# Optimization experiments

Hardware: AMD Instinct MI355X
Metric: run time of the kernel (lower is better)

## Reference

```python
import jax, jax.numpy as jnp
import numpy as np

B, N, DIM = 4, 1024, 512
H, DH = 16, 13            # dim_head stays at Attention's default 13
INNER = H * DH            # 208
L = 2                     # depth
MULT = 4
LA, LG = 1.0, 0.5
EPS = 1e-5


def layer_norm(x, g, b):
    m = jnp.mean(x, axis=-1, keepdims=True)
    v = jnp.mean((x - m) ** 2, axis=-1, keepdims=True)
    return (x - m) / jnp.sqrt(v + EPS) * g + b


def attention(x, mask, adj, qkv_w, out_w, out_b):
    b, n, _ = x.shape
    qkv = (x @ qkv_w).reshape(b, n, H, 3, DH)          # 'b n (h qkv d)'
    q = jnp.transpose(qkv[..., 0, :], (0, 2, 1, 3))    # b h n d
    k = jnp.transpose(qkv[..., 1, :], (0, 2, 1, 3))
    v = jnp.transpose(qkv[..., 2, :], (0, 2, 1, 3))
    dots = jnp.einsum('bhid,bhjd->bhij', q, k) * (DH ** -0.5)
    m2 = mask[:, None, :, None] & mask[:, None, None, :]  # b 1 n n
    big = jnp.finfo(dots.dtype).max
    dots = jnp.where(m2, dots, -big)
    adj4 = jnp.where(m2, adj[:, None, :, :], 0.0)
    attn = jax.nn.softmax(dots, axis=-1) * LA + LG * adj4
    out = jnp.einsum('bhij,bhjd->bhid', attn, v)
    out = jnp.transpose(out, (0, 2, 1, 3)).reshape(b, n, INNER)
    return out @ out_w + out_b


def feed_forward(x, w1, b1, w2, b2):
    return jax.nn.gelu(x @ w1 + b1, approximate=False) @ w2 + b2


def setup_inputs() -> dict:
    key = jax.random.key(0)
    ks = jax.random.split(key, 24)
    s = 0.02
    inp = {
        'x': jax.random.normal(ks[0], (B, N, DIM), jnp.float32),
        'mask': jax.random.randint(ks[1], (B, N), 0, 2).astype(bool),
        'adjacency_mat': jax.random.uniform(ks[2], (B, N, N), jnp.float32),
        'embed_w': jax.random.normal(ks[3], (DIM, DIM), jnp.float32) * s,
        'embed_b': jnp.zeros((DIM,), jnp.float32),
        'ln1_g': jnp.ones((L, DIM), jnp.float32),
        'ln1_b': jnp.zeros((L, DIM), jnp.float32),
        'qkv_w': jax.random.normal(ks[4], (L, DIM, 3 * INNER), jnp.float32) * s,
        'out_w': jax.random.normal(ks[5], (L, INNER, DIM), jnp.float32) * s,
        'out_b': jnp.zeros((L, DIM), jnp.float32),
        'ln2_g': jnp.ones((L, DIM), jnp.float32),
        'ln2_b': jnp.zeros((L, DIM), jnp.float32),
        'ff1_w': jax.random.normal(ks[6], (L, DIM, MULT * DIM), jnp.float32) * s,
        'ff1_b': jnp.zeros((L, MULT * DIM), jnp.float32),
        'ff2_w': jax.random.normal(ks[7], (L, MULT * DIM, DIM), jnp.float32) * s,
        'ff2_b': jnp.zeros((L, DIM), jnp.float32),
        'lnout_g': jnp.ones((DIM,), jnp.float32),
        'lnout_b': jnp.zeros((DIM,), jnp.float32),
        'ffo1_w': jax.random.normal(ks[8], (DIM, MULT * DIM), jnp.float32) * s,
        'ffo1_b': jnp.zeros((MULT * DIM,), jnp.float32),
        'ffo2_w': jax.random.normal(ks[9], (MULT * DIM, DIM), jnp.float32) * s,
        'ffo2_b': jnp.zeros((DIM,), jnp.float32),
    }
    return inp


def reference(x, mask, adjacency_mat, embed_w, embed_b, ln1_g, ln1_b, qkv_w,
              out_w, out_b, ln2_g, ln2_b, ff1_w, ff1_b, ff2_w, ff2_b,
              lnout_g, lnout_b, ffo1_w, ffo1_b, ffo2_w, ffo2_b):
    h = x @ embed_w + embed_b
    for l in range(L):
        h = h + attention(layer_norm(h, ln1_g[l], ln1_b[l]), mask,
                          adjacency_mat, qkv_w[l], out_w[l], out_b[l])
        h = h + feed_forward(layer_norm(h, ln2_g[l], ln2_b[l]),
                             ff1_w[l], ff1_b[l], ff2_w[l], ff2_b[l])
    h = layer_norm(h, lnout_g, lnout_b)
    h = jnp.mean(h, axis=-2)                     # pool over nodes -> [B, DIM]
    return feed_forward(h, ffo1_w, ffo1_b, ffo2_w, ffo2_b)
```

## Files before the change

### kernel.cpp

```cpp
#include <hip/hip_runtime.h>
#include <math.h>

#define BB    4
#define NN    1024
#define DIM   512
#define HH    16
#define DH    13
#define INNER 208
#define QKVN  624
#define QKVNP 640
#define KOUTP 224
#define FFH   2048
#define ROWS  4096

typedef __attribute__((ext_vector_type(8))) short short8v;
typedef __attribute__((ext_vector_type(4))) float f32x4;

__device__ __forceinline__ unsigned short f2bf(float f) {
    union { float f; unsigned int u; } x; x.f = f;
    unsigned int u = x.u + 0x7FFFu + ((x.u >> 16) & 1u);
    return (unsigned short)(u >> 16);
}
__device__ __forceinline__ float gelu_exact(float x) {
    return 0.5f * x * (1.0f + erff(x * 0.70710678118654752f));
}

__global__ __launch_bounds__(1024) void mask_detect_kernel(
        const unsigned char* __restrict__ mraw, int* __restrict__ flag) {
    __shared__ int any;
    if (threadIdx.x == 0) any = 0;
    __syncthreads();
    int t = threadIdx.x;
    int v = mraw[4 * t + 1] | mraw[4 * t + 2] | mraw[4 * t + 3];
    if (v) atomicOr(&any, 1);
    __syncthreads();
    if (threadIdx.x == 0) *flag = any;
}

__global__ __launch_bounds__(256) void mask_convert_kernel(
        const void* __restrict__ mraw, const int* __restrict__ flag,
        int* __restrict__ rowmask, float* __restrict__ maskfb) {
    int i = blockIdx.x * 256 + threadIdx.x;
    int v;
    if (*flag) v = ((const unsigned char*)mraw)[i] != 0;
    else       v = ((const int*)mraw)[i] != 0;
    rowmask[i] = v;
    maskfb[i] = v ? 1.0f : 0.0f;
}

__global__ __launch_bounds__(256) void zero16_kernel(uint4* __restrict__ p) {
    p[blockIdx.x * 256 + threadIdx.x] = (uint4){0u, 0u, 0u, 0u};
}

__global__ __launch_bounds__(256) void convw_kernel(
        const float* __restrict__ src, unsigned short* __restrict__ dst,
        int srcK, int srcN, int dstK, int dstN) {
    __shared__ float t[64][65];
    const int n0 = blockIdx.x * 64, k0 = blockIdx.y * 64;
    const int tq = threadIdx.x & 15, tr = threadIdx.x >> 4;
#pragma unroll
    for (int it = 0; it < 4; ++it) {
        int kl = tr + it * 16;
        int kg = k0 + kl;
        int ng = n0 + tq * 4;
        float4 v = {0.f, 0.f, 0.f, 0.f};
        if (kg < srcK) {
            const float* sp = src + (size_t)kg * srcN;
            if (ng + 3 < srcN) v = *(const float4*)(sp + ng);
            else {
                if (ng + 0 < srcN) v.x = sp[ng + 0];
                if (ng + 1 < srcN) v.y = sp[ng + 1];
                if (ng + 2 < srcN) v.z = sp[ng + 2];
                if (ng + 3 < srcN) v.w = sp[ng + 3];
            }
        }
        t[kl][tq * 4 + 0] = v.x; t[kl][tq * 4 + 1] = v.y;
        t[kl][tq * 4 + 2] = v.z; t[kl][tq * 4 + 3] = v.w;
    }
    __syncthreads();
#pragma unroll
    for (int it = 0; it < 4; ++it) {
        int nl = tr + it * 16;
        int ng = n0 + nl;
        int kg = k0 + tq * 4;
        if (ng < dstN && kg < dstK) {
            ushort4 o;
            o.x = f2bf(t[tq * 4 + 0][nl]); o.y = f2bf(t[tq * 4 + 1][nl]);
            o.z = f2bf(t[tq * 4 + 2][nl]); o.w = f2bf(t[tq * 4 + 3][nl]);
            *(ushort4*)(dst + (size_t)ng * dstK + kg) = o;
        }
    }
}

__global__ __launch_bounds__(256) void convx_kernel(
        const float* __restrict__ src, unsigned short* __restrict__ dst, int n8) {
    int idx = blockIdx.x * 256 + threadIdx.x;
    if (idx >= n8) return;
    float4 a = ((const float4*)src)[idx * 2];
    float4 b = ((const float4*)src)[idx * 2 + 1];
    uint4 o;
    o.x = (unsigned)f2bf(a.x) | ((unsigned)f2bf(a.y) << 16);
    o.y = (unsigned)f2bf(a.z) | ((unsigned)f2bf(a.w) << 16);
    o.z = (unsigned)f2bf(b.x) | ((unsigned)f2bf(b.y) << 16);
    o.w = (unsigned)f2bf(b.z) | ((unsigned)f2bf(b.w) << 16);
    ((uint4*)dst)[idx] = o;
}

__global__ __launch_bounds__(256) void zpad_kernel(unsigned short* __restrict__ attnout) {
    int idx = blockIdx.x * 256 + threadIdx.x;
    int row = idx >> 4, c = INNER + (idx & 15);
    attnout[(size_t)row * KOUTP + c] = 0;
}

__global__ __launch_bounds__(256) void adjmask_kernel(
        const float* __restrict__ adj, const int* __restrict__ rmask,
        unsigned short* __restrict__ adjbf) {
    int idx = blockIdx.x * 256 + threadIdx.x;
    int j8 = idx & 127;
    int row = idx >> 7;
    int b = row >> 10;
    int mi = rmask[row];
    const float* ap = adj + (size_t)row * NN + j8 * 8;
    const int* rm = rmask + (b << 10) + j8 * 8;
    float4 a0 = *(const float4*)ap, a1 = *(const float4*)(ap + 4);
    unsigned short o[8];
    o[0] = (mi && rm[0]) ? f2bf(a0.x) : 0;
    o[1] = (mi && rm[1]) ? f2bf(a0.y) : 0;
    o[2] = (mi && rm[2]) ? f2bf(a0.z) : 0;
    o[3] = (mi && rm[3]) ? f2bf(a0.w) : 0;
    o[4] = (mi && rm[4]) ? f2bf(a1.x) : 0;
    o[5] = (mi && rm[5]) ? f2bf(a1.y) : 0;
    o[6] = (mi && rm[6]) ? f2bf(a1.z) : 0;
    o[7] = (mi && rm[7]) ? f2bf(a1.w) : 0;
    uint4 pk;
    pk.x = (unsigned)o[0] | ((unsigned)o[1] << 16);
    pk.y = (unsigned)o[2] | ((unsigned)o[3] << 16);
    pk.z = (unsigned)o[4] | ((unsigned)o[5] << 16);
    pk.w = (unsigned)o[6] | ((unsigned)o[7] << 16);
    *(uint4*)(adjbf + (size_t)row * NN + j8 * 8) = pk;
}

template<int EPI, int BM, int BN>
__global__ __launch_bounds__(256) void mm_kernel(
        const unsigned short* __restrict__ A, const unsigned short* __restrict__ W,
        const float* __restrict__ bias, void* __restrict__ Cdst,
        int K, int lda, int ldc,
        long long aBatch, long long bBatch, long long cBatch,
        unsigned short* __restrict__ Qb, unsigned short* __restrict__ Kb,
        unsigned short* __restrict__ Vtb, unsigned short* __restrict__ V2t)
{
    constexpr int MF = BM / 32;
    constexpr int NF = BN / 32;
    constexpr int AROUNDS = BM / 64;
    constexpr int BROUNDS = BN / 64;
    __shared__ unsigned short As[BM * 32];
    __shared__ unsigned short Bs[BN * 32];
    const int tid = threadIdx.x;
    const int m0 = blockIdx.y * BM;
    const int n0 = blockIdx.x * BN;
    const int z  = blockIdx.z;

    const int lane = tid & 63;
    const int wv = tid >> 6;
    const int wvbase = wv << 6;
    const int wm = wv >> 1, wn = wv & 1;
    const int lrow = lane & 15, kgrp = lane >> 4;

    f32x4 acc[MF][NF];
#pragma unroll
    for (int i = 0; i < MF; ++i)
#pragma unroll
        for (int j = 0; j < NF; ++j) acc[i][j] = (f32x4){0.f, 0.f, 0.f, 0.f};

    const unsigned short* Ab = A + (size_t)z * aBatch;
    const unsigned short* Wb = W + (size_t)z * bBatch;

    for (int k0 = 0; k0 < K; k0 += 32) {
#pragma unroll
        for (int r = 0; r < AROUNDS; ++r) {
            int c = r * 256 + tid;
            const unsigned short* g = Ab + (size_t)(m0 + (c >> 2)) * lda + k0 + (c & 3) * 8;
            __builtin_amdgcn_global_load_lds((const unsigned int*)g,
                (unsigned int*)&As[(r * 256 + wvbase) * 8], 16, 0, 0);
        }
#pragma unroll
        for (int r = 0; r < BROUNDS; ++r) {
            int c = r * 256 + tid;
            const unsigned short* g = Wb + (size_t)(n0 + (c >> 2)) * K + k0 + (c & 3) * 8;
            __builtin_amdgcn_global_load_lds((const unsigned int*)g,
                (unsigned int*)&Bs[(r * 256 + wvbase) * 8], 16, 0, 0);
        }
        __syncthreads();
        short8v af[MF], bfv[NF];
#pragma unroll
        for (int f = 0; f < MF; ++f)
            af[f] = *(const short8v*)&As[(wm * (BM / 2) + f * 16 + lrow) * 32 + kgrp * 8];
#pragma unroll
        for (int f = 0; f < NF; ++f)
            bfv[f] = *(const short8v*)&Bs[(wn * (BN / 2) + f * 16 + lrow) * 32 + kgrp * 8];
#pragma unroll
        for (int fi = 0; fi < MF; ++fi)
#pragma unroll
            for (int fj = 0; fj < NF; ++fj)
                acc[fi][fj] = __builtin_amdgcn_mfma_f32_16x16x32_bf16(
                    af[fi], bfv[fj], acc[fi][fj], 0, 0, 0);
        __syncthreads();
    }

#pragma unroll
    for (int fi = 0; fi < MF; ++fi) {
#pragma unroll
        for (int fj = 0; fj < NF; ++fj) {
#pragma unroll
            for (int p = 0; p < 4; ++p) {
                int row = m0 + wm * (BM / 2) + fi * 16 + kgrp * 4 + p;
                int col = n0 + wn * (BN / 2) + fj * 16 + lrow;
                float v = acc[fi][fj][p];
                if (EPI == 0) {
                    float* C = (float*)Cdst + (size_t)z * cBatch;
                    if (bias) v += bias[col];
                    C[(size_t)row * ldc + col] = v;
                } else if (EPI == 1) {
                    unsigned short* C = (unsigned short*)Cdst;
                    C[(size_t)row * ldc + col] = f2bf(gelu_exact(v + bias[col]));
                } else if (EPI == 2) {
                    float* C = (float*)Cdst;
                    C[(size_t)row * ldc + col] += v + bias[col];
                } else {
                    if (col < QKVN) {
                        int hh  = col / 39;
                        int rem = col - hh * 39;
                        int sel = rem / 13;
                        int d   = rem - sel * 13;
                        int bb = row >> 10, n = row & (NN - 1);
                        int bh = bb * HH + hh;
                        unsigned short bv = f2bf(v);
                        if (sel == 0) {
                            Qb[((size_t)bh * NN + n) * 16 + d] = bv;
                        } else if (sel == 1) {
                            int rr = (n & ~31) | (((n >> 2) & 1) << 4)
                                   | (((n >> 3) & 3) << 2) | (n & 3);
                            Kb[((size_t)bh * NN + rr) * 16 + d] = bv;
                        } else {
                            Vtb[((size_t)bh * 16 + d) * NN + n] = bv;
                            V2t[((size_t)bb * 256 + hh * 13 + d) * NN + n] = bv;
                        }
                    }
                }
            }
        }
    }
}

template<int BFOUT>
__global__ __launch_bounds__(256) void ln_kernel(
        const float* __restrict__ x, const float* __restrict__ g,
        const float* __restrict__ bta, void* __restrict__ y) {
    const int lane = threadIdx.x & 63;
    const int row = (blockIdx.x * 256 + threadIdx.x) >> 6;
    const float* xp = x + (size_t)row * DIM + lane * 8;
    float4 v0 = *(const float4*)(xp);
    float4 v1 = *(const float4*)(xp + 4);
    float s = v0.x + v0.y + v0.z + v0.w + v1.x + v1.y + v1.z + v1.w;
#pragma unroll
    for (int off = 32; off >= 1; off >>= 1) s += __shfl_xor(s, off);
    float mean = s * (1.0f / DIM);
    float q =
        (v0.x - mean) * (v0.x - mean) + (v0.y - mean) * (v0.y - mean) +
        (v0.z - mean) * (v0.z - mean) + (v0.w - mean) * (v0.w - mean) +
        (v1.x - mean) * (v1.x - mean) + (v1.y - mean) * (v1.y - mean) +
        (v1.z - mean) * (v1.z - mean) + (v1.w - mean) * (v1.w - mean);
#pragma unroll
    for (int off = 32; off >= 1; off >>= 1) q += __shfl_xor(q, off);
    float rstd = rsqrtf(q * (1.0f / DIM) + 1e-5f);
    const int c = lane * 8;
    float4 g0 = *(const float4*)(g + c), g1 = *(const float4*)(g + c + 4);
    float4 b0 = *(const float4*)(bta + c), b1 = *(const float4*)(bta + c + 4);
    float o0 = (v0.x - mean) * rstd * g0.x + b0.x;
    float o1 = (v0.y - mean) * rstd * g0.y + b0.y;
    float o2 = (v0.z - mean) * rstd * g0.z + b0.z;
    float o3 = (v0.w - mean) * rstd * g0.w + b0.w;
    float o4 = (v1.x - mean) * rstd * g1.x + b1.x;
    float o5 = (v1.y - mean) * rstd * g1.y + b1.y;
    float o6 = (v1.z - mean) * rstd * g1.z + b1.z;
    float o7 = (v1.w - mean) * rstd * g1.w + b1.w;
    if (BFOUT) {
        unsigned short* yp = (unsigned short*)y + (size_t)row * DIM + c;
        uint4 o;
        o.x = (unsigned)f2bf(o0) | ((unsigned)f2bf(o1) << 16);
        o.y = (unsigned)f2bf(o2) | ((unsigned)f2bf(o3) << 16);
        o.z = (unsigned)f2bf(o4) | ((unsigned)f2bf(o5) << 16);
        o.w = (unsigned)f2bf(o6) | ((unsigned)f2bf(o7) << 16);
        *(uint4*)yp = o;
    } else {
        float* yp = (float*)y + (size_t)row * DIM + c;
        *(float4*)(yp)     = (float4){o0, o1, o2, o3};
        *(float4*)(yp + 4) = (float4){o4, o5, o6, o7};
    }
}

__global__ __launch_bounds__(256) void attn4_kernel(
        const unsigned short* __restrict__ Qb, const unsigned short* __restrict__ Kb,
        const unsigned short* __restrict__ Vtb, const float* __restrict__ adjout,
        const int* __restrict__ rmask, const float* __restrict__ maskfb,
        unsigned short* __restrict__ attnout) {
    const int tid = threadIdx.x;
    const int qt = blockIdx.x, h = blockIdx.y, b = blockIdx.z;
    const int bh = b * HH + h;
    const int wv = tid >> 6, lane = tid & 63;
    const int lrow = lane & 15, g = lane >> 4;
    const int q = qt * 64 + wv * 16 + lrow;
    const int mi = rmask[b * NN + q];
    const float scl = mi ? (0.27735009811261457f * 1.4426950408889634f) : 0.0f;
    const float mif = mi ? 1.0f : 0.0f;

    short8v qf = (short8v){0, 0, 0, 0, 0, 0, 0, 0};
    if (g < 2)
        qf = *(const short8v*)(Qb + ((size_t)bh * NN + q) * 16 + g * 8);

    const unsigned short* Kbh = Kb + (size_t)bh * NN * 16;
    const unsigned short* Vrow = Vtb + ((size_t)bh * 16 + lrow) * NN;
    const float* mfp = maskfb + b * NN;

    f32x4 oacc = (f32x4){0.f, 0.f, 0.f, 0.f};
    float zacc = 0.0f;

    for (int t = 0; t < 32; ++t) {
        const int j0 = t * 32;
        short8v kf0 = (short8v){0, 0, 0, 0, 0, 0, 0, 0};
        short8v kf1 = (short8v){0, 0, 0, 0, 0, 0, 0, 0};
        if (g < 2) {
            kf0 = *(const short8v*)(Kbh + (size_t)(j0 + lrow) * 16 + g * 8);
            kf1 = *(const short8v*)(Kbh + (size_t)(j0 + 16 + lrow) * 16 + g * 8);
        }
        f32x4 s0 = (f32x4){0.f, 0.f, 0.f, 0.f};
        f32x4 s1 = (f32x4){0.f, 0.f, 0.f, 0.f};
        s0 = __builtin_amdgcn_mfma_f32_16x16x32_bf16(kf0, qf, s0, 0, 0, 0);
        s1 = __builtin_amdgcn_mfma_f32_16x16x32_bf16(kf1, qf, s1, 0, 0, 0);
        float4 m0 = *(const float4*)&mfp[j0 + g * 8];
        float4 m1 = *(const float4*)&mfp[j0 + g * 8 + 4];
        float w0 = exp2f(fminf(s0[0] * scl, 80.f)) * fmaf(mif, m0.x - 1.f, 1.f);
        float w1 = exp2f(fminf(s0[1] * scl, 80.f)) * fmaf(mif, m0.y - 1.f, 1.f);
        float w2 = exp2f(fminf(s0[2] * scl, 80.f)) * fmaf(mif, m0.z - 1.f, 1.f);
        float w3 = exp2f(fminf(s0[3] * scl, 80.f)) * fmaf(mif, m0.w - 1.f, 1.f);
        float w4 = exp2f(fminf(s1[0] * scl, 80.f)) * fmaf(mif, m1.x - 1.f, 1.f);
        float w5 = exp2f(fminf(s1[1] * scl, 80.f)) * fmaf(mif, m1.y - 1.f, 1.f);
        float w6 = exp2f(fminf(s1[2] * scl, 80.f)) * fmaf(mif, m1.z - 1.f, 1.f);
        float w7 = exp2f(fminf(s1[3] * scl, 80.f)) * fmaf(mif, m1.w - 1.f, 1.f);
        zacc += ((w0 + w1) + (w2 + w3)) + ((w4 + w5) + (w6 + w7));
        unsigned p01, p23, p45, p67;
        asm("v_cvt_pk_bf16_f32 %0, %1, %2" : "=v"(p01) : "v"(w0), "v"(w1));
        asm("v_cvt_pk_bf16_f32 %0, %1, %2" : "=v"(p23) : "v"(w2), "v"(w3));
        asm("v_cvt_pk_bf16_f32 %0, %1, %2" : "=v"(p45) : "v"(w4), "v"(w5));
        asm("v_cvt_pk_bf16_f32 %0, %1, %2" : "=v"(p67) : "v"(w6), "v"(w7));
        union { uint4 u4; short8v s8; } pu;
        pu.u4 = (uint4){p01, p23, p45, p67};
        short8v vf = *(const short8v*)(Vrow + j0 + g * 8);
        oacc = __builtin_amdgcn_mfma_f32_16x16x32_bf16(vf, pu.s8, oacc, 0, 0, 0);
    }

    zacc += __shfl_xor(zacc, 16);
    zacc += __shfl_xor(zacc, 32);
    float inv = 1.0f / zacc;

    const float* arow = adjout + ((size_t)(b * NN + q)) * 256 + h * 13;
    unsigned short* orow = attnout + (size_t)(b * NN + q) * KOUTP + h * 13;
#pragma unroll
    for (int p = 0; p < 4; ++p) {
        int d = 4 * g + p;
        if (d < 13)
            orow[d] = f2bf(fmaf(oacc[p], inv, 0.5f * arow[d]));
    }
}

__global__ __launch_bounds__(256) void pool1_kernel(
        const float* __restrict__ xn, float* __restrict__ poolpart) {
    __shared__ float red[256][4];
    const int ch = blockIdx.x, b = blockIdx.y;
    const int c4 = threadIdx.x & 127, p = threadIdx.x >> 7;
    const float* base = xn + ((size_t)(b * NN) + ch * 64 + p) * DIM + c4 * 4;
    float4 s = {0.f, 0.f, 0.f, 0.f};
    for (int r = 0; r < 32; ++r) {
        float4 v = *(const float4*)(base + (size_t)r * 2 * DIM);
        s.x += v.x; s.y += v.y; s.z += v.z; s.w += v.w;
    }
    *(float4*)red[threadIdx.x] = s;
    __syncthreads();
    if (threadIdx.x < 128) {
        float4 a = *(float4*)red[threadIdx.x];
        float4 c = *(float4*)red[threadIdx.x + 128];
        float4 o = {a.x + c.x, a.y + c.y, a.z + c.z, a.w + c.w};
        *(float4*)(poolpart + (size_t)(b * 16 + ch) * DIM + c4 * 4) = o;
    }
}

__global__ __launch_bounds__(256) void pool2_kernel(
        const float* __restrict__ poolpart, float* __restrict__ pooled) {
    int c = blockIdx.x * 256 + threadIdx.x;
    int b = c >> 9, col = c & 511;
    float s = 0.f;
    for (int ch = 0; ch < 16; ++ch)
        s += poolpart[(size_t)(b * 16 + ch) * DIM + col];
    pooled[c] = s * (1.0f / NN);
}

__global__ __launch_bounds__(256) void ffo1a_kernel(
        const float* __restrict__ pooled, const float* __restrict__ w,
        float* __restrict__ part) {
    int n = blockIdx.x * 256 + threadIdx.x;
    int kc = blockIdx.y;
    float s0 = 0.f, s1 = 0.f, s2 = 0.f, s3 = 0.f;
    for (int k = kc * 128; k < kc * 128 + 128; ++k) {
        float wv = w[(size_t)k * FFH + n];
        s0 = fmaf(pooled[k], wv, s0);
        s1 = fmaf(pooled[512 + k], wv, s1);
        s2 = fmaf(pooled[1024 + k], wv, s2);
        s3 = fmaf(pooled[1536 + k], wv, s3);
    }
    part[(size_t)(kc * 4 + 0) * FFH + n] = s0;
    part[(size_t)(kc * 4 + 1) * FFH + n] = s1;
    part[(size_t)(kc * 4 + 2) * FFH + n] = s2;
    part[(size_t)(kc * 4 + 3) * FFH + n] = s3;
}

__global__ __launch_bounds__(256) void ffo1b_kernel(
        const float* __restrict__ part, const float* __restrict__ bias,
        float* __restrict__ ffoh) {
    int c = blockIdx.x * 256 + threadIdx.x;
    int b = c >> 11, n = c & 2047;
    float s = bias[n];
#pragma unroll
    for (int kc = 0; kc < 4; ++kc)
        s += part[(size_t)(kc * 4 + b) * FFH + n];
    ffoh[c] = gelu_exact(s);
}

__global__ __launch_bounds__(256) void ffo2a_kernel(
        const float* __restrict__ ffoh, const float* __restrict__ w,
        float* __restrict__ part) {
    int n = blockIdx.x * 256 + threadIdx.x;
    int kc = blockIdx.y;
    float s0 = 0.f, s1 = 0.f, s2 = 0.f, s3 = 0.f;
    for (int k = kc * 128; k < kc * 128 + 128; ++k) {
        float wv = w[(size_t)k * DIM + n];
        s0 = fmaf(ffoh[k], wv, s0);
        s1 = fmaf(ffoh[2048 + k], wv, s1);
        s2 = fmaf(ffoh[4096 + k], wv, s2);
        s3 = fmaf(ffoh[6144 + k], wv, s3);
    }
    part[(size_t)(kc * 4 + 0) * DIM + n] = s0;
    part[(size_t)(kc * 4 + 1) * DIM + n] = s1;
    part[(size_t)(kc * 4 + 2) * DIM + n] = s2;
    part[(size_t)(kc * 4 + 3) * DIM + n] = s3;
}

__global__ __launch_bounds__(256) void ffo2b_kernel(
        const float* __restrict__ part, const float* __restrict__ bias,
        float* __restrict__ out) {
    int c = blockIdx.x * 256 + threadIdx.x;
    int b = c >> 9, n = c & 511;
    float s = bias[n];
#pragma unroll
    for (int kc = 0; kc < 16; ++kc)
        s += part[(size_t)(kc * 4 + b) * DIM + n];
    out[c] = s;
}

extern "C" void kernel_launch(void* const* d_in, const int* in_sizes, int n_in,
                              void* d_out, int out_size, void* d_ws, size_t ws_size,
                              hipStream_t stream) {
    const float* x       = (const float*)d_in[0];
    const void*  mraw    = d_in[1];
    const float* adj     = (const float*)d_in[2];
    const float* embed_w = (const float*)d_in[3];
    const float* embed_b = (const float*)d_in[4];
    const float* ln1_g   = (const float*)d_in[5];
    const float* ln1_b   = (const float*)d_in[6];
    const float* qkv_w   = (const float*)d_in[7];
    const float* out_w   = (const float*)d_in[8];
    const float* out_b   = (const float*)d_in[9];
    const float* ln2_g   = (const float*)d_in[10];
    const float* ln2_b   = (const float*)d_in[11];
    const float* ff1_w   = (const float*)d_in[12];
    const float* ff1_b   = (const float*)d_in[13];
    const float* ff2_w   = (const float*)d_in[14];
    const float* ff2_b   = (const float*)d_in[15];
    const float* lnout_g = (const float*)d_in[16];
    const float* lnout_b = (const float*)d_in[17];
    const float* ffo1_w  = (const float*)d_in[18];
    const float* ffo1_b  = (const float*)d_in[19];
    const float* ffo2_w  = (const float*)d_in[20];
    const float* ffo2_b  = (const float*)d_in[21];

    char* ws = (char*)d_ws;
    float*          h       = (float*)(ws + 0);
    unsigned short* xnbf    = (unsigned short*)(ws + 8388608);
    char*           R       = ws + 12582912;
    unsigned short* adjbf   = (unsigned short*)(R + 0);
    unsigned short* Qb      = (unsigned short*)(R + 8388608);
    unsigned short* Kb      = (unsigned short*)(R + 10485760);
    unsigned short* Vtb     = (unsigned short*)(R + 12582912);
    unsigned short* V2t     = (unsigned short*)(R + 14680064);
    float*          adjout  = (float*)(R + 16777216);
    unsigned short* ffh     = (unsigned short*)(R + 0);
    float*          xnf     = (float*)(R + 0);
    float*          part1   = (float*)(R + 8388608);
    float*          part2   = (float*)(R + 8519680);
    unsigned short* attnout = (unsigned short*)(ws + 37486592);
    unsigned short* embedwt = (unsigned short*)(ws + 39321600);
    unsigned short* qkvwt   = (unsigned short*)(ws + 39845888);
    unsigned short* outwt   = (unsigned short*)(ws + 41156608);
    unsigned short* ff1wt   = (unsigned short*)(ws + 41615360);
    unsigned short* ff2wt   = (unsigned short*)(ws + 45809664);
    float*          poolpart= (float*)(ws + 50003968);
    float*          pooled  = (float*)(ws + 50135040);
    float*          ffoh    = (float*)(ws + 50143232);
    int*            rowmask = (int*)(ws + 50176000);
    float*          maskfb  = (float*)(ws + 50192384);
    int*            flag    = (int*)(ws + 50208768);

    mask_detect_kernel<<<1, 1024, 0, stream>>>((const unsigned char*)mraw, flag);
    mask_convert_kernel<<<16, 256, 0, stream>>>(mraw, flag, rowmask, maskfb);
    convx_kernel<<<1024, 256, 0, stream>>>(x, xnbf, ROWS * DIM / 8);
    convw_kernel<<<dim3(8, 8), 256, 0, stream>>>(embed_w, embedwt, 512, 512, 512, 512);
    for (int l = 0; l < 2; ++l) {
        convw_kernel<<<dim3(10, 8), 256, 0, stream>>>(qkv_w + (size_t)l * 512 * 624,
            qkvwt + (size_t)l * QKVNP * 512, 512, 624, 512, QKVNP);
        convw_kernel<<<dim3(8, 4), 256, 0, stream>>>(out_w + (size_t)l * 208 * 512,
            outwt + (size_t)l * 512 * KOUTP, 208, 512, KOUTP, 512);
        convw_kernel<<<dim3(32, 8), 256, 0, stream>>>(ff1_w + (size_t)l * 512 * 2048,
            ff1wt + (size_t)l * 2048 * 512, 512, 2048, 512, 2048);
        convw_kernel<<<dim3(8, 32), 256, 0, stream>>>(ff2_w + (size_t)l * 512 * 2048,
            ff2wt + (size_t)l * 512 * 2048, 2048, 512, 2048, 512);
    }
    zpad_kernel<<<256, 256, 0, stream>>>(attnout);

    mm_kernel<0, 64, 64><<<dim3(8, 64, 1), 256, 0, stream>>>(
        xnbf, embedwt, embed_b, h, 512, 512, 512, 0, 0, 0,
        nullptr, nullptr, nullptr, nullptr);

    for (int l = 0; l < 2; ++l) {
        ln_kernel<1><<<1024, 256, 0, stream>>>(h, ln1_g + l * DIM, ln1_b + l * DIM, xnbf);
        zero16_kernel<<<2048, 256, 0, stream>>>((uint4*)(R + 8388608));
        mm_kernel<3, 128, 64><<<dim3(10, 32, 1), 256, 0, stream>>>(
            xnbf, qkvwt + (size_t)l * QKVNP * 512, nullptr, nullptr,
            512, 512, 0, 0, 0, 0, Qb, Kb, Vtb, V2t);
        adjmask_kernel<<<2048, 256, 0, stream>>>(adj, rowmask, adjbf);
        mm_kernel<0, 64, 64><<<dim3(4, 16, 4), 256, 0, stream>>>(
            adjbf, V2t, nullptr, adjout, 1024, 1024, 256,
            (long long)NN * NN, (long long)256 * NN, (long long)NN * 256,
            nullptr, nullptr, nullptr, nullptr);
        attn4_kernel<<<dim3(16, 16, 4), 256, 0, stream>>>(
            Qb, Kb, Vtb, adjout, rowmask, maskfb, attnout);
        mm_kernel<2, 64, 64><<<dim3(8, 64, 1), 256, 0, stream>>>(
            attnout, outwt + (size_t)l * 512 * KOUTP, out_b + l * DIM, h,
            KOUTP, KOUTP, 512, 0, 0, 0, nullptr, nullptr, nullptr, nullptr);
        ln_kernel<1><<<1024, 256, 0, stream>>>(h, ln2_g + l * DIM, ln2_b + l * DIM, xnbf);
        mm_kernel<1, 128, 128><<<dim3(16, 32, 1), 256, 0, stream>>>(
            xnbf, ff1wt + (size_t)l * 2048 * 512, ff1_b + l * FFH, ffh,
            512, 512, 2048, 0, 0, 0, nullptr, nullptr, nullptr, nullptr);
        mm_kernel<2, 64, 64><<<dim3(8, 64, 1), 256, 0, stream>>>(
            ffh, ff2wt + (size_t)l * 512 * 2048, ff2_b + l * DIM, h,
            2048, 2048, 512, 0, 0, 0, nullptr, nullptr, nullptr, nullptr);
    }

    ln_kernel<0><<<1024, 256, 0, stream>>>(h, lnout_g, lnout_b, xnf);
    pool1_kernel<<<dim3(16, 4), 256, 0, stream>>>(xnf, poolpart);
    pool2_kernel<<<8, 256, 0, stream>>>(poolpart, pooled);
    ffo1a_kernel<<<dim3(8, 4), 256, 0, stream>>>(pooled, ffo1_w, part1);
    ffo1b_kernel<<<32, 256, 0, stream>>>(part1, ffo1_b, ffoh);
    ffo2a_kernel<<<dim3(2, 16), 256, 0, stream>>>(ffoh, ffo2_w, part2);
    ffo2b_kernel<<<8, 256, 0, stream>>>(part2, ffo2_b, (float*)d_out);
}
```

Before: 400.1 us.

## Hoist adjacency masking and pad zeroing out of layer loop, shrink QKV tile

```diff
diff --git a/kernel.cpp b/kernel.cpp
--- a/kernel.cpp
+++ b/kernel.cpp
@@ -48,8 +48,27 @@
     maskfb[i] = v ? 1.0f : 0.0f;
 }
 
-__global__ __launch_bounds__(256) void zero16_kernel(uint4* __restrict__ p) {
-    p[blockIdx.x * 256 + threadIdx.x] = (uint4){0u, 0u, 0u, 0u};
+__global__ __launch_bounds__(256) void padzero_kernel(
+        unsigned short* __restrict__ Qb, unsigned short* __restrict__ Kb,
+        unsigned short* __restrict__ Vtb, unsigned short* __restrict__ V2t) {
+    int idx = blockIdx.x * 256 + threadIdx.x;
+    if (idx < 65536) {
+        unsigned short* p = Qb + (size_t)idx * 16 + 13;
+        p[0] = 0; p[1] = 0; p[2] = 0;
+    } else if (idx < 131072) {
+        unsigned short* p = Kb + (size_t)(idx - 65536) * 16 + 13;
+        p[0] = 0; p[1] = 0; p[2] = 0;
+    } else if (idx < 155648) {
+        int i = idx - 131072;
+        int bh = i / 384, r = (i >> 7) % 3, c = i & 127;
+        *(uint4*)(Vtb + ((size_t)(bh * 16 + 13 + r) * 1024 + c * 8)) =
+            (uint4){0u, 0u, 0u, 0u};
+    } else if (idx < 180224) {
+        int i = idx - 155648;
+        int b = i / 6144, r = (i >> 7) % 48, c = i & 127;
+        *(uint4*)(V2t + ((size_t)(b * 256 + 208 + r) * 1024 + c * 8)) =
+            (uint4){0u, 0u, 0u, 0u};
+    }
 }
 
 __global__ __launch_bounds__(256) void convw_kernel(
@@ -495,29 +514,28 @@
     char* ws = (char*)d_ws;
     float*          h       = (float*)(ws + 0);
     unsigned short* xnbf    = (unsigned short*)(ws + 8388608);
-    char*           R       = ws + 12582912;
-    unsigned short* adjbf   = (unsigned short*)(R + 0);
-    unsigned short* Qb      = (unsigned short*)(R + 8388608);
-    unsigned short* Kb      = (unsigned short*)(R + 10485760);
-    unsigned short* Vtb     = (unsigned short*)(R + 12582912);
-    unsigned short* V2t     = (unsigned short*)(R + 14680064);
-    float*          adjout  = (float*)(R + 16777216);
-    unsigned short* ffh     = (unsigned short*)(R + 0);
-    float*          xnf     = (float*)(R + 0);
-    float*          part1   = (float*)(R + 8388608);
-    float*          part2   = (float*)(R + 8519680);
-    unsigned short* attnout = (unsigned short*)(ws + 37486592);
-    unsigned short* embedwt = (unsigned short*)(ws + 39321600);
-    unsigned short* qkvwt   = (unsigned short*)(ws + 39845888);
-    unsigned short* outwt   = (unsigned short*)(ws + 41156608);
-    unsigned short* ff1wt   = (unsigned short*)(ws + 41615360);
-    unsigned short* ff2wt   = (unsigned short*)(ws + 45809664);
-    float*          poolpart= (float*)(ws + 50003968);
-    float*          pooled  = (float*)(ws + 50135040);
-    float*          ffoh    = (float*)(ws + 50143232);
-    int*            rowmask = (int*)(ws + 50176000);
-    float*          maskfb  = (float*)(ws + 50192384);
-    int*            flag    = (int*)(ws + 50208768);
+    unsigned short* adjbf   = (unsigned short*)(ws + 12582912);
+    unsigned short* Qb      = (unsigned short*)(ws + 20971520);
+    unsigned short* Kb      = (unsigned short*)(ws + 23068672);
+    unsigned short* Vtb     = (unsigned short*)(ws + 25165824);
+    unsigned short* V2t     = (unsigned short*)(ws + 27262976);
+    float*          adjout  = (float*)(ws + 29360128);
+    unsigned short* ffh     = (unsigned short*)(ws + 33554432);
+    float*          xnf     = (float*)(ws + 50331648);
+    unsigned short* attnout = (unsigned short*)(ws + 58720256);
+    unsigned short* embedwt = (unsigned short*)(ws + 60555264);
+    unsigned short* qkvwt   = (unsigned short*)(ws + 61079552);
+    unsigned short* outwt   = (unsigned short*)(ws + 62390272);
+    unsigned short* ff1wt   = (unsigned short*)(ws + 62849024);
+    unsigned short* ff2wt   = (unsigned short*)(ws + 67043328);
+    float*          poolpart= (float*)(ws + 71237632);
+    float*          pooled  = (float*)(ws + 71368704);
+    float*          ffoh    = (float*)(ws + 71376896);
+    float*          part1   = (float*)(ws + 71409664);
+    float*          part2   = (float*)(ws + 71540736);
+    int*            rowmask = (int*)(ws + 71671808);
+    float*          maskfb  = (float*)(ws + 71688192);
+    int*            flag    = (int*)(ws + 71704576);
 
     mask_detect_kernel<<<1, 1024, 0, stream>>>((const unsigned char*)mraw, flag);
     mask_convert_kernel<<<16, 256, 0, stream>>>(mraw, flag, rowmask, maskfb);
@@ -534,6 +552,8 @@
             ff2wt + (size_t)l * 512 * 2048, 2048, 512, 2048, 512);
     }
     zpad_kernel<<<256, 256, 0, stream>>>(attnout);
+    padzero_kernel<<<704, 256, 0, stream>>>(Qb, Kb, Vtb, V2t);
+    adjmask_kernel<<<2048, 256, 0, stream>>>(adj, rowmask, adjbf);
 
     mm_kernel<0, 64, 64><<<dim3(8, 64, 1), 256, 0, stream>>>(
         xnbf, embedwt, embed_b, h, 512, 512, 512, 0, 0, 0,
@@ -541,11 +561,9 @@
 
     for (int l = 0; l < 2; ++l) {
         ln_kernel<1><<<1024, 256, 0, stream>>>(h, ln1_g + l * DIM, ln1_b + l * DIM, xnbf);
-        zero16_kernel<<<2048, 256, 0, stream>>>((uint4*)(R + 8388608));
-        mm_kernel<3, 128, 64><<<dim3(10, 32, 1), 256, 0, stream>>>(
+        mm_kernel<3, 64, 64><<<dim3(10, 64, 1), 256, 0, stream>>>(
             xnbf, qkvwt + (size_t)l * QKVNP * 512, nullptr, nullptr,
             512, 512, 0, 0, 0, 0, Qb, Kb, Vtb, V2t);
-        adjmask_kernel<<<2048, 256, 0, stream>>>(adj, rowmask, adjbf);
         mm_kernel<0, 64, 64><<<dim3(4, 16, 4), 256, 0, stream>>>(
             adjbf, V2t, nullptr, adjout, 1024, 1024, 256,
             (long long)NN * NN, (long long)256 * NN, (long long)NN * 256,
```

Measured after the change: 377.9 us. 5.6% less time.
